# Performance work log

Measured on AMD Instinct MI355X. Metric: run time of the kernel, lower is better.

## Reference

```python
import jax, jax.numpy as jnp
import numpy as np

B, S, H = 4, 8192, 768
NH, HD = 12, 64          # num_heads, head_size
M = 64                   # projection_dim = min(256, HD)
EPS = 1e-6

def setup_inputs() -> dict:
    key = jax.random.key(0)
    ks = jax.random.split(key, 10)
    scale_w = 0.02
    scale_p = 1.0 / np.sqrt(HD)
    return {
        'hidden_states': jax.random.normal(ks[0], (B, S, H), jnp.float32),
        'Wq': jax.random.normal(ks[1], (H, H), jnp.float32) * scale_w,
        'bq': jnp.zeros((H,), jnp.float32),
        'Wk': jax.random.normal(ks[2], (H, H), jnp.float32) * scale_w,
        'bk': jnp.zeros((H,), jnp.float32),
        'Wv': jax.random.normal(ks[3], (H, H), jnp.float32) * scale_w,
        'bv': jnp.zeros((H,), jnp.float32),
        'Wo': jax.random.normal(ks[4], (H, H), jnp.float32) * scale_w,
        'bo': jnp.zeros((H,), jnp.float32),
        'projection_matrix': jax.random.normal(ks[5], (NH, HD, M), jnp.float32) * scale_p,
    }

def reference(hidden_states, Wq, bq, Wk, bk, Wv, bv, Wo, bo, projection_matrix):
    b, s, h = hidden_states.shape
    def heads(x):  # [b,s,h] -> [b,nh,s,hd]
        return x.reshape(b, s, NH, HD).transpose(0, 2, 1, 3)
    q = heads(hidden_states @ Wq + bq)
    k = heads(hidden_states @ Wk + bk)
    v = heads(hidden_states @ Wv + bv)
    # random-feature projection + stabilized exp feature map
    qp = jnp.einsum('bhnd,hdm->bhnm', q, projection_matrix)
    kp = jnp.einsum('bhnd,hdm->bhnm', k, projection_matrix)
    qp = jnp.exp(qp - jnp.max(qp, axis=-1, keepdims=True))
    kp = jnp.exp(kp - jnp.max(kp, axis=-1, keepdims=True))
    # O(n) linear attention: kv summary [b,h,m,hd]
    kv = jnp.einsum('bhnm,bhnd->bhmd', kp, v)
    qkv = jnp.einsum('bhnm,bhmd->bhnd', qp, kv)
    k_sum = jnp.sum(kp, axis=2)                      # [b,h,m]
    normalizer = jnp.einsum('bhnm,bhm->bhn', qp, k_sum)[..., None]
    ctx = qkv / (normalizer + EPS)
    ctx = ctx.transpose(0, 2, 1, 3).reshape(b, s, NH * HD)
    return ctx @ Wo + bo
```

## Files before the change

kernel.cpp:

```cpp
#include <hip/hip_runtime.h>
#include <hip/hip_bf16.h>


#define S_    8192
#define H_    768
#define NH_   12
#define EPS_  1e-6f

typedef unsigned short U16;
typedef short bf16x8 __attribute__((ext_vector_type(8)));
typedef float f32x4  __attribute__((ext_vector_type(4)));

__device__ __forceinline__ U16 f2b(float x) {
  unsigned u = __float_as_uint(x);
  return (U16)((u + 0x7fffu + ((u >> 16) & 1u)) >> 16);
}
__device__ __forceinline__ float b2f(U16 h) {
  return __uint_as_float(((unsigned)h) << 16);
}
__device__ __forceinline__ void gl2lds16(const void* g, void* l) {
  __builtin_amdgcn_global_load_lds(
      (const __attribute__((address_space(1))) void*)g,
      (__attribute__((address_space(3))) void*)l, 16, 0, 0);
}

__global__ void zero_f32(float* __restrict__ p, int n) {
  int i = blockIdx.x * 256 + threadIdx.x;
  if (i < n) p[i] = 0.f;
}

__global__ void cvt_f32_bf16(const float* __restrict__ src, U16* __restrict__ hi, int n4) {
  int i = blockIdx.x * 256 + threadIdx.x;
  if (i >= n4) return;
  float4 x = ((const float4*)src)[i];
  ushort4 h;
  h.x = f2b(x.x); h.y = f2b(x.y); h.z = f2b(x.z); h.w = f2b(x.w);
  ((ushort4*)hi)[i] = h;
}

__global__ void fold_proj(const float* __restrict__ Wq, const float* __restrict__ bq,
                          const float* __restrict__ Wk, const float* __restrict__ bk,
                          const float* __restrict__ P,
                          float* __restrict__ Wqp, float* __restrict__ bqp,
                          float* __restrict__ Wkp, float* __restrict__ bkp) {
  __shared__ float Pl[64 * 64];
  __shared__ float WL[4 * 64];
  int h = blockIdx.y, kc = blockIdx.x, tid = threadIdx.x;
  const float* W  = blockIdx.z ? Wk : Wq;
  const float* bb = blockIdx.z ? bk : bq;
  float* Wout = blockIdx.z ? Wkp : Wqp;
  float* bout = blockIdx.z ? bkp : bqp;
  const float4* P4 = (const float4*)(P + (size_t)h * 4096);
#pragma unroll
  for (int i = 0; i < 4; ++i) ((float4*)Pl)[tid + i * 256] = P4[tid + i * 256];
  WL[tid] = W[(size_t)(kc * 4 + (tid >> 6)) * H_ + h * 64 + (tid & 63)];
  __syncthreads();
  int kl = tid >> 6, m = tid & 63;
  float acc = 0.f;
#pragma unroll
  for (int d = 0; d < 64; ++d) acc += WL[kl * 64 + d] * Pl[d * 64 + m];
  Wout[(size_t)(kc * 4 + kl) * H_ + h * 64 + m] = acc;
  if (kc == 0 && tid < 64) {
    float a2 = 0.f;
    for (int d = 0; d < 64; ++d) a2 += bb[h * 64 + d] * Pl[d * 64 + tid];
    bout[h * 64 + tid] = a2;
  }
}

__global__ void build_cat(const float* __restrict__ Wqp, const float* __restrict__ Wkp,
                          const float* __restrict__ Wv,  const float* __restrict__ Wo,
                          U16* __restrict__ WcatH, U16* __restrict__ WoTH) {
  int k = blockIdx.x * 256 + threadIdx.x;
  int r = blockIdx.y;
  float v; U16* dh; size_t off;
  if (r < 768)       { v = Wqp[(size_t)k * H_ + r];          off = (size_t)r * H_ + k;          dh = WcatH; }
  else if (r < 1536) { v = Wkp[(size_t)k * H_ + (r - 768)];  off = (size_t)r * H_ + k;          dh = WcatH; }
  else if (r < 2304) { v = Wv [(size_t)k * H_ + (r - 1536)]; off = (size_t)r * H_ + k;          dh = WcatH; }
  else               { v = Wo [(size_t)k * H_ + (r - 2304)]; off = (size_t)(r - 2304) * H_ + k; dh = WoTH; }
  dh[off] = f2b(v);
}

__global__ void build_bias(const float* __restrict__ bqp, const float* __restrict__ bkp,
                           const float* __restrict__ bv, float* __restrict__ biasC) {
  int i = blockIdx.x * 256 + threadIdx.x;
  if (i >= 2304) return;
  biasC[i] = i < 768 ? bqp[i] : (i < 1536 ? bkp[i - 768] : bv[i - 1536]);
}

__global__ __launch_bounds__(256, 4) void gemm_qkv(
    const U16* __restrict__ Ahi, const U16* __restrict__ Bhi,
    const float* __restrict__ bias,
    U16* __restrict__ qp, U16* __restrict__ kpT, U16* __restrict__ vT) {
  __shared__ __align__(16) U16 Us[2 * 128 * 32];
  const int tid = threadIdx.x, w = tid >> 6, lane = tid & 63;
  const int quad = lane >> 4, l16 = lane & 15;
  const int rowA0 = blockIdx.y * 128, colB0 = blockIdx.x * 128;
  const int wm = w & 1, wn = w >> 1;
  const int K = 768;
  f32x4 acc[4][4] = {};
  const U16* srcs[4];
  unsigned ldsoff[4];
#pragma unroll
  for (int t = 0; t < 4; ++t) {
    int c = w * 4 + t, cc = c & 7, buf = c >> 3;
    const U16* base = buf ? Bhi : Ahi;
    int r0 = buf ? colB0 : rowA0;
    srcs[t] = base + (size_t)(r0 + cc * 16 + (lane >> 2)) * K + (lane & 3) * 8;
    ldsoff[t] = c * 512;
  }
  for (int k0 = 0; k0 < K; k0 += 32) {
#pragma unroll
    for (int t = 0; t < 4; ++t) gl2lds16(srcs[t] + k0, &Us[ldsoff[t]]);
    __syncthreads();
    bf16x8 ah[4];
#pragma unroll
    for (int i = 0; i < 4; ++i)
      ah[i] = *(const bf16x8*)&Us[(wm * 64 + i * 16 + l16) * 32 + quad * 8];
#pragma unroll
    for (int j = 0; j < 4; ++j) {
      bf16x8 bh = *(const bf16x8*)&Us[4096 + (wn * 64 + j * 16 + l16) * 32 + quad * 8];
#pragma unroll
      for (int i = 0; i < 4; ++i)
        acc[i][j] = __builtin_amdgcn_mfma_f32_16x16x32_bf16(ah[i], bh, acc[i][j], 0, 0, 0);
    }
    __syncthreads();
  }
  const int col64 = colB0 + wn * 64;
  float bj[4];
#pragma unroll
  for (int j = 0; j < 4; ++j) bj[j] = bias[col64 + j * 16 + l16];
  if (col64 < 768) {
    const int h = col64 >> 6;
#pragma unroll
    for (int i = 0; i < 4; ++i) {
#pragma unroll
      for (int r = 0; r < 4; ++r) {
        int row = rowA0 + wm * 64 + i * 16 + quad * 4 + r;
        float v0 = acc[i][0][r] + bj[0], v1 = acc[i][1][r] + bj[1];
        float v2 = acc[i][2][r] + bj[2], v3 = acc[i][3][r] + bj[3];
        float mx = fmaxf(fmaxf(v0, v1), fmaxf(v2, v3));
        mx = fmaxf(mx, __shfl_xor(mx, 1));
        mx = fmaxf(mx, __shfl_xor(mx, 2));
        mx = fmaxf(mx, __shfl_xor(mx, 4));
        mx = fmaxf(mx, __shfl_xor(mx, 8));
        int b = row >> 13, s = row & 8191;
        size_t base = ((size_t)(b * NH_ + h) * S_ + s) * 64 + l16;
        qp[base +  0] = f2b(__expf(v0 - mx));
        qp[base + 16] = f2b(__expf(v1 - mx));
        qp[base + 32] = f2b(__expf(v2 - mx));
        qp[base + 48] = f2b(__expf(v3 - mx));
      }
    }
  } else {
    const int isv = col64 >= 1536;
    const int h = (col64 - (isv ? 1536 : 768)) >> 6;
    U16* dstT = isv ? vT : kpT;
#pragma unroll
    for (int i = 0; i < 4; ++i) {
      float er[4][4];
#pragma unroll
      for (int r = 0; r < 4; ++r) {
        float v0 = acc[i][0][r] + bj[0], v1 = acc[i][1][r] + bj[1];
        float v2 = acc[i][2][r] + bj[2], v3 = acc[i][3][r] + bj[3];
        if (!isv) {
          float mx = fmaxf(fmaxf(v0, v1), fmaxf(v2, v3));
          mx = fmaxf(mx, __shfl_xor(mx, 1));
          mx = fmaxf(mx, __shfl_xor(mx, 2));
          mx = fmaxf(mx, __shfl_xor(mx, 4));
          mx = fmaxf(mx, __shfl_xor(mx, 8));
          v0 = __expf(v0 - mx); v1 = __expf(v1 - mx);
          v2 = __expf(v2 - mx); v3 = __expf(v3 - mx);
        }
        er[0][r] = v0; er[1][r] = v1; er[2][r] = v2; er[3][r] = v3;
      }
      int n = rowA0 + wm * 64 + i * 16 + quad * 4;
      int b = n >> 13, s = n & 8191;
      int bh = b * NH_ + h;
#pragma unroll
      for (int j = 0; j < 4; ++j) {
        ushort4 o;
        o.x = f2b(er[j][0]); o.y = f2b(er[j][1]);
        o.z = f2b(er[j][2]); o.w = f2b(er[j][3]);
        *(ushort4*)&dstT[((size_t)bh * 64 + j * 16 + l16) * S_ + s] = o;
      }
    }
  }
}

__global__ __launch_bounds__(256, 4) void kv_accum_mfma(
    const U16* __restrict__ kpT, const U16* __restrict__ vT,
    float* __restrict__ kvT) {
  __shared__ __align__(16) U16 Us[2 * 64 * 64];
  const int tid = threadIdx.x, w = tid >> 6, lane = tid & 63;
  const int quad = lane >> 4, l16 = lane & 15;
  const int bh = blockIdx.y;
  const int n0 = blockIdx.x * 1024;
  const U16* srcs[4];
  unsigned ldsoff[4];
#pragma unroll
  for (int t = 0; t < 4; ++t) {
    int c = w * 4 + t, buf = c >> 3;
    int r = (c & 7) * 8 + (lane >> 3);
    const U16* base = buf ? kpT : vT;
    srcs[t] = base + ((size_t)bh * 64 + r) * S_ + n0 + (lane & 7) * 8;
    ldsoff[t] = buf * 4096 + (c & 7) * 512;
  }
  f32x4 acc[4] = {};
  float ks[4] = {0.f, 0.f, 0.f, 0.f};
  for (int nc = 0; nc < 1024; nc += 64) {
#pragma unroll
    for (int t = 0; t < 4; ++t) gl2lds16(srcs[t] + nc, &Us[ldsoff[t]]);
    __syncthreads();
#pragma unroll
    for (int k0 = 0; k0 < 64; k0 += 32) {
      bf16x8 av = *(const bf16x8*)&Us[(w * 16 + l16) * 64 + k0 + quad * 8];
#pragma unroll
      for (int j = 0; j < 4; ++j) {
        bf16x8 bk = *(const bf16x8*)&Us[4096 + (j * 16 + l16) * 64 + k0 + quad * 8];
        if (w == 0) {
#pragma unroll
          for (int e = 0; e < 8; ++e) ks[j] += b2f((U16)bk[e]);
        }
        acc[j] = __builtin_amdgcn_mfma_f32_16x16x32_bf16(av, bk, acc[j], 0, 0, 0);
      }
    }
    __syncthreads();
  }
#pragma unroll
  for (int j = 0; j < 4; ++j)
#pragma unroll
    for (int r = 0; r < 4; ++r) {
      int d = w * 16 + quad * 4 + r;
      atomicAdd(&kvT[((size_t)bh * 80 + d) * 64 + j * 16 + l16], acc[j][r]);
    }
  if (w == 0) {
#pragma unroll
    for (int j = 0; j < 4; ++j) {
      ks[j] += __shfl_xor(ks[j], 16);
      ks[j] += __shfl_xor(ks[j], 32);
    }
    if (lane < 16) {
#pragma unroll
      for (int j = 0; j < 4; ++j)
        atomicAdd(&kvT[((size_t)bh * 80 + 64) * 64 + j * 16 + lane], ks[j]);
    }
  }
}

__global__ __launch_bounds__(256) void ctx_gemm_k(
    const U16* __restrict__ qp, const float* __restrict__ kvT,
    U16* __restrict__ ctx) {
  __shared__ __align__(16) U16 As[128 * 64];
  __shared__ __align__(16) U16 Bs[80 * 64];
  int bh = blockIdx.y, row0 = blockIdx.x * 128;
  int tid = threadIdx.x, w = tid >> 6, lane = tid & 63;
  int quad = lane >> 4, l16 = lane & 15;
  const U16* Ab = qp + ((size_t)bh * S_ + row0) * 64;
#pragma unroll
  for (int t = 0; t < 4; ++t) {
    int cb = (w * 4 + t) * 64;
    gl2lds16(Ab + (size_t)(cb + lane) * 8, &As[cb * 8]);
  }
  const float4* kv4 = (const float4*)(kvT + (size_t)bh * 5120);
#pragma unroll
  for (int t = 0; t < 5; ++t) {
    int idx = t * 256 + tid;
    float4 f = kv4[idx];
    ushort4 o;
    o.x = f2b(f.x); o.y = f2b(f.y); o.z = f2b(f.z); o.w = f2b(f.w);
    *(ushort4*)&Bs[idx * 4] = o;
  }
  __syncthreads();
  f32x4 acc[2][5] = {};
#pragma unroll
  for (int k0 = 0; k0 < 64; k0 += 32) {
    bf16x8 a[2], fb[5];
#pragma unroll
    for (int i = 0; i < 2; ++i)
      a[i] = *(const bf16x8*)&As[(w * 32 + i * 16 + l16) * 64 + k0 + quad * 8];
#pragma unroll
    for (int j = 0; j < 5; ++j)
      fb[j] = *(const bf16x8*)&Bs[(j * 16 + l16) * 64 + k0 + quad * 8];
#pragma unroll
    for (int j = 0; j < 5; ++j)
#pragma unroll
      for (int i = 0; i < 2; ++i)
        acc[i][j] = __builtin_amdgcn_mfma_f32_16x16x32_bf16(a[i], fb[j], acc[i][j], 0, 0, 0);
  }
  int b = bh / NH_, h = bh - b * NH_;
#pragma unroll
  for (int i = 0; i < 2; ++i) {
#pragma unroll
    for (int r = 0; r < 4; ++r) {
      int s = row0 + w * 32 + i * 16 + quad * 4 + r;
      float nv = __shfl(acc[i][4][r], lane & 48);
      float inv = 1.f / (nv + EPS_);
      size_t base = ((size_t)b * S_ + s) * H_ + h * 64;
#pragma unroll
      for (int j = 0; j < 4; ++j)
        ctx[base + j * 16 + l16] = f2b(acc[i][j][r] * inv);
    }
  }
}

__global__ __launch_bounds__(256, 4) void gemm_out(
    const U16* __restrict__ Ahi, const U16* __restrict__ Bhi,
    const float* __restrict__ bias, float* __restrict__ C, int K, int ldc) {
  __shared__ __align__(16) U16 Us[2 * 128 * 32];
  const int tid = threadIdx.x, w = tid >> 6, lane = tid & 63;
  const int quad = lane >> 4, l16 = lane & 15;
  const int rowA0 = blockIdx.y * 128, colB0 = blockIdx.x * 128;
  const int wm = w & 1, wn = w >> 1;
  f32x4 acc[4][4] = {};
  const U16* srcs[4];
  unsigned ldsoff[4];
#pragma unroll
  for (int t = 0; t < 4; ++t) {
    int c = w * 4 + t, cc = c & 7, buf = c >> 3;
    const U16* base = buf ? Bhi : Ahi;
    int r0 = buf ? colB0 : rowA0;
    srcs[t] = base + (size_t)(r0 + cc * 16 + (lane >> 2)) * K + (lane & 3) * 8;
    ldsoff[t] = c * 512;
  }
  for (int k0 = 0; k0 < K; k0 += 32) {
#pragma unroll
    for (int t = 0; t < 4; ++t) gl2lds16(srcs[t] + k0, &Us[ldsoff[t]]);
    __syncthreads();
    bf16x8 ah[4];
#pragma unroll
    for (int i = 0; i < 4; ++i)
      ah[i] = *(const bf16x8*)&Us[(wm * 64 + i * 16 + l16) * 32 + quad * 8];
#pragma unroll
    for (int j = 0; j < 4; ++j) {
      bf16x8 bh = *(const bf16x8*)&Us[4096 + (wn * 64 + j * 16 + l16) * 32 + quad * 8];
#pragma unroll
      for (int i = 0; i < 4; ++i)
        acc[i][j] = __builtin_amdgcn_mfma_f32_16x16x32_bf16(ah[i], bh, acc[i][j], 0, 0, 0);
    }
    __syncthreads();
  }
#pragma unroll
  for (int i = 0; i < 4; ++i) {
    int row = rowA0 + wm * 64 + i * 16 + quad * 4;
#pragma unroll
    for (int j = 0; j < 4; ++j) {
      int col = colB0 + wn * 64 + j * 16 + l16;
      float bvv = bias[col];
#pragma unroll
      for (int r = 0; r < 4; ++r)
        C[(size_t)(row + r) * ldc + col] = acc[i][j][r] + bvv;
    }
  }
}

extern "C" void kernel_launch(void* const* d_in, const int* in_sizes, int n_in,
                              void* d_out, int out_size, void* d_ws, size_t ws_size,
                              hipStream_t stream) {
  const float* hs = (const float*)d_in[0];
  const float* Wq = (const float*)d_in[1];
  const float* bq = (const float*)d_in[2];
  const float* Wk = (const float*)d_in[3];
  const float* bk = (const float*)d_in[4];
  const float* Wv = (const float*)d_in[5];
  const float* bv = (const float*)d_in[6];
  const float* Wo = (const float*)d_in[7];
  const float* bo = (const float*)d_in[8];
  const float* P  = (const float*)d_in[9];
  float* out = (float*)d_out;

  char* ws = (char*)d_ws;
  size_t off = 0;
  auto alloc = [&](size_t bytes) -> void* {
    void* p = ws + off;
    off = (off + bytes + 255) & ~(size_t)255;
    return p;
  };
  U16*   hs_hi = (U16*)alloc(50331648);
  float* WqpF  = (float*)alloc(2359296);
  float* WkpF  = (float*)alloc(2359296);
  float* bqpF  = (float*)alloc(3072);
  float* bkpF  = (float*)alloc(3072);
  U16*   WcatH = (U16*)alloc(3538944);
  U16*   WoTH  = (U16*)alloc(1179648);
  float* biasC = (float*)alloc(9216);
  U16*   qp    = (U16*)alloc(50331648);
  U16*   kpT   = (U16*)alloc(50331648);
  U16*   vT    = (U16*)alloc(50331648);
  float* kvT   = (float*)alloc(983040);
  U16*   ctx   = hs_hi;

  zero_f32<<<dim3(960), dim3(256), 0, stream>>>(kvT, 245760);
  cvt_f32_bf16<<<dim3(24576), dim3(256), 0, stream>>>(hs, hs_hi, 6291456);
  fold_proj<<<dim3(192, 12, 2), dim3(256), 0, stream>>>(Wq, bq, Wk, bk, P, WqpF, bqpF, WkpF, bkpF);
  build_cat<<<dim3(3, 3072), dim3(256), 0, stream>>>(WqpF, WkpF, Wv, Wo, WcatH, WoTH);
  build_bias<<<dim3(9), dim3(256), 0, stream>>>(bqpF, bkpF, bv, biasC);
  gemm_qkv<<<dim3(18, 256), dim3(256), 0, stream>>>(hs_hi, WcatH, biasC, qp, kpT, vT);
  kv_accum_mfma<<<dim3(8, 48), dim3(256), 0, stream>>>(kpT, vT, kvT);
  ctx_gemm_k<<<dim3(64, 48), dim3(256), 0, stream>>>(qp, kvT, ctx);
  gemm_out<<<dim3(6, 256), dim3(256), 0, stream>>>(ctx, WoTH, bo, out, 768, 768);
}
```

Baseline: 504.2 us.

## Rewrite QKV and output GEMMs with 256x256 tiles and double-buffered swizzled LDS

Both projection GEMMs move from 128x128 tiles with single-buffered K=32 steps to 512-thread blocks computing 256x256 tiles. Each K=64 step is double-buffered in LDS with an XOR-swizzled layout, explicit vmcnt waits, raw barriers and setprio around the MFMA bursts. Blocks are remapped through a 1D grid swizzle so neighbouring blocks share operand tiles in L2. The kv accumulation kernel is split across twice as many sequence chunks for more parallelism. The aim is higher data reuse per block and overlap of global loads with MFMA work, at the cost of more registers and LDS per block and fewer resident blocks.

```diff
diff --git a/kernel.cpp b/kernel.cpp
--- a/kernel.cpp
+++ b/kernel.cpp
@@ -87,44 +87,78 @@
   biasC[i] = i < 768 ? bqp[i] : (i < 1536 ? bkp[i - 768] : bv[i - 1536]);
 }
 
-__global__ __launch_bounds__(256, 4) void gemm_qkv(
+__global__ __launch_bounds__(512, 2) void gemm_qkv(
     const U16* __restrict__ Ahi, const U16* __restrict__ Bhi,
     const float* __restrict__ bias,
     U16* __restrict__ qp, U16* __restrict__ kpT, U16* __restrict__ vT) {
-  __shared__ __align__(16) U16 Us[2 * 128 * 32];
+  __shared__ __align__(16) U16 Us[65536];
   const int tid = threadIdx.x, w = tid >> 6, lane = tid & 63;
   const int quad = lane >> 4, l16 = lane & 15;
-  const int rowA0 = blockIdx.y * 128, colB0 = blockIdx.x * 128;
-  const int wm = w & 1, wn = w >> 1;
-  const int K = 768;
-  f32x4 acc[4][4] = {};
-  const U16* srcs[4];
-  unsigned ldsoff[4];
-#pragma unroll
-  for (int t = 0; t < 4; ++t) {
-    int c = w * 4 + t, cc = c & 7, buf = c >> 3;
-    const U16* base = buf ? Bhi : Ahi;
-    int r0 = buf ? colB0 : rowA0;
-    srcs[t] = base + (size_t)(r0 + cc * 16 + (lane >> 2)) * K + (lane & 3) * 8;
-    ldsoff[t] = c * 512;
-  }
-  for (int k0 = 0; k0 < K; k0 += 32) {
-#pragma unroll
-    for (int t = 0; t < 4; ++t) gl2lds16(srcs[t] + k0, &Us[ldsoff[t]]);
-    __syncthreads();
-    bf16x8 ah[4];
-#pragma unroll
-    for (int i = 0; i < 4; ++i)
-      ah[i] = *(const bf16x8*)&Us[(wm * 64 + i * 16 + l16) * 32 + quad * 8];
-#pragma unroll
-    for (int j = 0; j < 4; ++j) {
-      bf16x8 bh = *(const bf16x8*)&Us[4096 + (wn * 64 + j * 16 + l16) * 32 + quad * 8];
-#pragma unroll
-      for (int i = 0; i < 4; ++i)
-        acc[i][j] = __builtin_amdgcn_mfma_f32_16x16x32_bf16(ah[i], bh, acc[i][j], 0, 0, 0);
-    }
-    __syncthreads();
-  }
+  const int id = blockIdx.x;
+  const int swz = (id & 7) * 144 + (id >> 3);
+  const int mt = swz & 127, nt = swz >> 7;
+  const int rowA0 = mt * 256, colB0 = nt * 256;
+  const int wm = w >> 2, wn = w & 3;
+  const int srow = w * 8 + (lane >> 3);
+  const int kch = ((lane & 7) ^ (lane >> 3)) * 8;
+  const U16* As = Ahi + (size_t)(rowA0 + srow) * H_ + kch;
+  const U16* Bs = Bhi + (size_t)(colB0 + srow) * H_ + kch;
+  const unsigned lb = (unsigned)(w * 8) * 64;
+
+  f32x4 acc[8][4] = {};
+
+  auto stage = [&](int kt, int bi) {
+    const U16* ap = As + kt * 64;
+    const U16* bp = Bs + kt * 64;
+    unsigned ub = (unsigned)bi * 32768u + lb;
+#pragma unroll
+    for (int q = 0; q < 4; ++q) {
+      gl2lds16(ap + (size_t)(q * 64) * H_, &Us[ub + q * 4096]);
+      gl2lds16(bp + (size_t)(q * 64) * H_, &Us[ub + 16384u + q * 4096]);
+    }
+  };
+
+  stage(0, 0);
+  stage(1, 1);
+  for (int t = 0; t < 12; ++t) {
+    const unsigned ab = (unsigned)(t & 1) * 32768u;
+    if (t < 11) asm volatile("s_waitcnt vmcnt(8)" ::: "memory");
+    else        asm volatile("s_waitcnt vmcnt(0)" ::: "memory");
+    __builtin_amdgcn_sched_barrier(0);
+    __builtin_amdgcn_s_barrier();
+    __builtin_amdgcn_sched_barrier(0);
+#pragma unroll
+    for (int ks = 0; ks < 2; ++ks) {
+      const int xo = ks * 4 + quad;
+#pragma unroll
+      for (int mh = 0; mh < 2; ++mh) {
+        bf16x8 ah[4], bh[4];
+#pragma unroll
+        for (int i = 0; i < 4; ++i) {
+          int row = wm * 128 + mh * 64 + i * 16 + l16;
+          ah[i] = *(const bf16x8*)&Us[ab + row * 64 + ((xo ^ (l16 & 7)) * 8)];
+        }
+#pragma unroll
+        for (int j = 0; j < 4; ++j) {
+          int row = wn * 64 + j * 16 + l16;
+          bh[j] = *(const bf16x8*)&Us[ab + 16384u + row * 64 + ((xo ^ (l16 & 7)) * 8)];
+        }
+        __builtin_amdgcn_s_setprio(1);
+#pragma unroll
+        for (int j = 0; j < 4; ++j)
+#pragma unroll
+          for (int i = 0; i < 4; ++i)
+            acc[mh * 4 + i][j] = __builtin_amdgcn_mfma_f32_16x16x32_bf16(
+                ah[i], bh[j], acc[mh * 4 + i][j], 0, 0, 0);
+        __builtin_amdgcn_s_setprio(0);
+      }
+    }
+    __builtin_amdgcn_sched_barrier(0);
+    __builtin_amdgcn_s_barrier();
+    __builtin_amdgcn_sched_barrier(0);
+    if (t + 2 < 12) stage(t + 2, t & 1);
+  }
+
   const int col64 = colB0 + wn * 64;
   float bj[4];
 #pragma unroll
@@ -132,12 +166,12 @@
   if (col64 < 768) {
     const int h = col64 >> 6;
 #pragma unroll
-    for (int i = 0; i < 4; ++i) {
+    for (int f = 0; f < 8; ++f) {
 #pragma unroll
       for (int r = 0; r < 4; ++r) {
-        int row = rowA0 + wm * 64 + i * 16 + quad * 4 + r;
-        float v0 = acc[i][0][r] + bj[0], v1 = acc[i][1][r] + bj[1];
-        float v2 = acc[i][2][r] + bj[2], v3 = acc[i][3][r] + bj[3];
+        int row = rowA0 + wm * 128 + f * 16 + quad * 4 + r;
+        float v0 = acc[f][0][r] + bj[0], v1 = acc[f][1][r] + bj[1];
+        float v2 = acc[f][2][r] + bj[2], v3 = acc[f][3][r] + bj[3];
         float mx = fmaxf(fmaxf(v0, v1), fmaxf(v2, v3));
         mx = fmaxf(mx, __shfl_xor(mx, 1));
         mx = fmaxf(mx, __shfl_xor(mx, 2));
@@ -156,12 +190,12 @@
     const int h = (col64 - (isv ? 1536 : 768)) >> 6;
     U16* dstT = isv ? vT : kpT;
 #pragma unroll
-    for (int i = 0; i < 4; ++i) {
+    for (int f = 0; f < 8; ++f) {
       float er[4][4];
 #pragma unroll
       for (int r = 0; r < 4; ++r) {
-        float v0 = acc[i][0][r] + bj[0], v1 = acc[i][1][r] + bj[1];
-        float v2 = acc[i][2][r] + bj[2], v3 = acc[i][3][r] + bj[3];
+        float v0 = acc[f][0][r] + bj[0], v1 = acc[f][1][r] + bj[1];
+        float v2 = acc[f][2][r] + bj[2], v3 = acc[f][3][r] + bj[3];
         if (!isv) {
           float mx = fmaxf(fmaxf(v0, v1), fmaxf(v2, v3));
           mx = fmaxf(mx, __shfl_xor(mx, 1));
@@ -173,7 +207,7 @@
         }
         er[0][r] = v0; er[1][r] = v1; er[2][r] = v2; er[3][r] = v3;
       }
-      int n = rowA0 + wm * 64 + i * 16 + quad * 4;
+      int n = rowA0 + wm * 128 + f * 16 + quad * 4;
       int b = n >> 13, s = n & 8191;
       int bh = b * NH_ + h;
 #pragma unroll
@@ -194,7 +228,7 @@
   const int tid = threadIdx.x, w = tid >> 6, lane = tid & 63;
   const int quad = lane >> 4, l16 = lane & 15;
   const int bh = blockIdx.y;
-  const int n0 = blockIdx.x * 1024;
+  const int n0 = blockIdx.x * 512;
   const U16* srcs[4];
   unsigned ldsoff[4];
 #pragma unroll
@@ -207,7 +241,7 @@
   }
   f32x4 acc[4] = {};
   float ks[4] = {0.f, 0.f, 0.f, 0.f};
-  for (int nc = 0; nc < 1024; nc += 64) {
+  for (int nc = 0; nc < 512; nc += 64) {
 #pragma unroll
     for (int t = 0; t < 4; ++t) gl2lds16(srcs[t] + nc, &Us[ldsoff[t]]);
     __syncthreads();
@@ -303,52 +337,87 @@
   }
 }
 
-__global__ __launch_bounds__(256, 4) void gemm_out(
+__global__ __launch_bounds__(512, 2) void gemm_out(
     const U16* __restrict__ Ahi, const U16* __restrict__ Bhi,
-    const float* __restrict__ bias, float* __restrict__ C, int K, int ldc) {
-  __shared__ __align__(16) U16 Us[2 * 128 * 32];
+    const float* __restrict__ bias, float* __restrict__ C) {
+  __shared__ __align__(16) U16 Us[65536];
   const int tid = threadIdx.x, w = tid >> 6, lane = tid & 63;
   const int quad = lane >> 4, l16 = lane & 15;
-  const int rowA0 = blockIdx.y * 128, colB0 = blockIdx.x * 128;
-  const int wm = w & 1, wn = w >> 1;
-  f32x4 acc[4][4] = {};
-  const U16* srcs[4];
-  unsigned ldsoff[4];
-#pragma unroll
-  for (int t = 0; t < 4; ++t) {
-    int c = w * 4 + t, cc = c & 7, buf = c >> 3;
-    const U16* base = buf ? Bhi : Ahi;
-    int r0 = buf ? colB0 : rowA0;
-    srcs[t] = base + (size_t)(r0 + cc * 16 + (lane >> 2)) * K + (lane & 3) * 8;
-    ldsoff[t] = c * 512;
-  }
-  for (int k0 = 0; k0 < K; k0 += 32) {
-#pragma unroll
-    for (int t = 0; t < 4; ++t) gl2lds16(srcs[t] + k0, &Us[ldsoff[t]]);
-    __syncthreads();
-    bf16x8 ah[4];
-#pragma unroll
-    for (int i = 0; i < 4; ++i)
-      ah[i] = *(const bf16x8*)&Us[(wm * 64 + i * 16 + l16) * 32 + quad * 8];
-#pragma unroll
-    for (int j = 0; j < 4; ++j) {
-      bf16x8 bh = *(const bf16x8*)&Us[4096 + (wn * 64 + j * 16 + l16) * 32 + quad * 8];
-#pragma unroll
-      for (int i = 0; i < 4; ++i)
-        acc[i][j] = __builtin_amdgcn_mfma_f32_16x16x32_bf16(ah[i], bh, acc[i][j], 0, 0, 0);
-    }
-    __syncthreads();
-  }
-#pragma unroll
-  for (int i = 0; i < 4; ++i) {
-    int row = rowA0 + wm * 64 + i * 16 + quad * 4;
+  const int id = blockIdx.x;
+  const int swz = (id & 7) * 48 + (id >> 3);
+  const int mt = swz & 127, nt = swz >> 7;
+  const int rowA0 = mt * 256, colB0 = nt * 256;
+  const int wm = w >> 2, wn = w & 3;
+  const int srow = w * 8 + (lane >> 3);
+  const int kch = ((lane & 7) ^ (lane >> 3)) * 8;
+  const U16* As = Ahi + (size_t)(rowA0 + srow) * H_ + kch;
+  const U16* Bs = Bhi + (size_t)(colB0 + srow) * H_ + kch;
+  const unsigned lb = (unsigned)(w * 8) * 64;
+
+  f32x4 acc[8][4] = {};
+
+  auto stage = [&](int kt, int bi) {
+    const U16* ap = As + kt * 64;
+    const U16* bp = Bs + kt * 64;
+    unsigned ub = (unsigned)bi * 32768u + lb;
+#pragma unroll
+    for (int q = 0; q < 4; ++q) {
+      gl2lds16(ap + (size_t)(q * 64) * H_, &Us[ub + q * 4096]);
+      gl2lds16(bp + (size_t)(q * 64) * H_, &Us[ub + 16384u + q * 4096]);
+    }
+  };
+
+  stage(0, 0);
+  stage(1, 1);
+  for (int t = 0; t < 12; ++t) {
+    const unsigned ab = (unsigned)(t & 1) * 32768u;
+    if (t < 11) asm volatile("s_waitcnt vmcnt(8)" ::: "memory");
+    else        asm volatile("s_waitcnt vmcnt(0)" ::: "memory");
+    __builtin_amdgcn_sched_barrier(0);
+    __builtin_amdgcn_s_barrier();
+    __builtin_amdgcn_sched_barrier(0);
+#pragma unroll
+    for (int ks = 0; ks < 2; ++ks) {
+      const int xo = ks * 4 + quad;
+#pragma unroll
+      for (int mh = 0; mh < 2; ++mh) {
+        bf16x8 ah[4], bh[4];
+#pragma unroll
+        for (int i = 0; i < 4; ++i) {
+          int row = wm * 128 + mh * 64 + i * 16 + l16;
+          ah[i] = *(const bf16x8*)&Us[ab + row * 64 + ((xo ^ (l16 & 7)) * 8)];
+        }
+#pragma unroll
+        for (int j = 0; j < 4; ++j) {
+          int row = wn * 64 + j * 16 + l16;
+          bh[j] = *(const bf16x8*)&Us[ab + 16384u + row * 64 + ((xo ^ (l16 & 7)) * 8)];
+        }
+        __builtin_amdgcn_s_setprio(1);
+#pragma unroll
+        for (int j = 0; j < 4; ++j)
+#pragma unroll
+          for (int i = 0; i < 4; ++i)
+            acc[mh * 4 + i][j] = __builtin_amdgcn_mfma_f32_16x16x32_bf16(
+                ah[i], bh[j], acc[mh * 4 + i][j], 0, 0, 0);
+        __builtin_amdgcn_s_setprio(0);
+      }
+    }
+    __builtin_amdgcn_sched_barrier(0);
+    __builtin_amdgcn_s_barrier();
+    __builtin_amdgcn_sched_barrier(0);
+    if (t + 2 < 12) stage(t + 2, t & 1);
+  }
+
+#pragma unroll
+  for (int f = 0; f < 8; ++f) {
+    int row = rowA0 + wm * 128 + f * 16 + quad * 4;
 #pragma unroll
     for (int j = 0; j < 4; ++j) {
       int col = colB0 + wn * 64 + j * 16 + l16;
       float bvv = bias[col];
 #pragma unroll
       for (int r = 0; r < 4; ++r)
-        C[(size_t)(row + r) * ldc + col] = acc[i][j][r] + bvv;
+        C[(size_t)(row + r) * H_ + col] = acc[f][j][r] + bvv;
     }
   }
 }
@@ -394,8 +463,8 @@
   fold_proj<<<dim3(192, 12, 2), dim3(256), 0, stream>>>(Wq, bq, Wk, bk, P, WqpF, bqpF, WkpF, bkpF);
   build_cat<<<dim3(3, 3072), dim3(256), 0, stream>>>(WqpF, WkpF, Wv, Wo, WcatH, WoTH);
   build_bias<<<dim3(9), dim3(256), 0, stream>>>(bqpF, bkpF, bv, biasC);
-  gemm_qkv<<<dim3(18, 256), dim3(256), 0, stream>>>(hs_hi, WcatH, biasC, qp, kpT, vT);
-  kv_accum_mfma<<<dim3(8, 48), dim3(256), 0, stream>>>(kpT, vT, kvT);
+  gemm_qkv<<<dim3(1152), dim3(512), 0, stream>>>(hs_hi, WcatH, biasC, qp, kpT, vT);
+  kv_accum_mfma<<<dim3(16, 48), dim3(256), 0, stream>>>(kpT, vT, kvT);
   ctx_gemm_k<<<dim3(64, 48), dim3(256), 0, stream>>>(qp, kvT, ctx);
-  gemm_out<<<dim3(6, 256), dim3(256), 0, stream>>>(ctx, WoTH, bo, out, 768, 768);
-}
+  gemm_out<<<dim3(384), dim3(512), 0, stream>>>(ctx, WoTH, bo, out);
+}
```

Result: no change. 506.0 us (+0.4%).
